# Optimization experiments

Measured on AMD Instinct MI355X. Metric: run time of the kernel, lower is better.

Reference implementation:

```python
import jax, jax.numpy as jnp
import numpy as np

BN_EPS = 1e-5


def setup_inputs() -> dict:
    key = jax.random.key(0)
    ks = jax.random.split(key, 12)
    N, K, C_IN, C_OUT = 50000, 16, 128, 128
    C2 = 2 * C_OUT
    return {
        "features": jax.random.normal(ks[0], (N, C_IN), dtype=jnp.float32),
        "neighbor_idx": jax.random.randint(ks[1], (N, K), 0, N, dtype=jnp.int64),
        "W1": jax.random.normal(ks[2], (C_IN, C2), dtype=jnp.float32) * 0.05,
        "b1": jax.random.normal(ks[3], (C2,), dtype=jnp.float32) * 0.05,
        "gamma": jax.random.uniform(ks[4], (C2,), dtype=jnp.float32, minval=0.5, maxval=1.5),
        "beta": jax.random.normal(ks[5], (C2,), dtype=jnp.float32) * 0.05,
        "run_mean": jax.random.normal(ks[6], (C2,), dtype=jnp.float32) * 0.05,
        "run_var": jax.random.uniform(ks[7], (C2,), dtype=jnp.float32, minval=0.5, maxval=1.5),
        "Ws": jax.random.normal(ks[8], (C2, C2), dtype=jnp.float32) * 0.05,
        "Wm": jax.random.normal(ks[9], (C2, C_OUT), dtype=jnp.float32) * 0.05,
        "bm": jax.random.normal(ks[10], (C_OUT,), dtype=jnp.float32) * 0.05,
    }


def reference(features, neighbor_idx, W1, b1, gamma, beta, run_mean, run_var, Ws, Wm, bm):
    # mlp1: Linear + ReLU (no BN)
    x = jax.nn.relu(features @ W1 + b1)                     # (N, 2C)
    # gather_neighbour: irregular index_select
    g = x[neighbor_idx]                                     # (N, k, 2C)
    # BatchNorm1d over channel dim (inference semantics, running stats)
    inv = gamma * jax.lax.rsqrt(run_var + BN_EPS)
    g = (g - run_mean) * inv + beta                         # (N, k, 2C)
    # AttentivePooling: per-neighbor score linear (no bias), softmax over k
    scores = jax.nn.softmax(g @ Ws, axis=1)                 # (N, k, 2C)
    feat = jnp.sum(scores * g, axis=1)                      # (N, 2C)
    return feat @ Wm + bm                                   # (N, C_out)
```

## Files before the change

kernel.cpp:

```cpp
#include <hip/hip_runtime.h>
#include <cstddef>

#define C_IN  128
#define C2    256
#define C_OUT 128
#define KNBR  16

typedef unsigned short u16;
typedef __attribute__((ext_vector_type(8))) short bf16x8;
typedef __attribute__((ext_vector_type(4))) float f32x4;

__device__ __forceinline__ float bf2f(u16 h) {
    return __uint_as_float(((unsigned int)h) << 16);
}
__device__ __forceinline__ u16 f2bf(float x) {
    unsigned int u = __float_as_uint(x);
    return (u16)((u + 0x7fffu + ((u >> 16) & 1u)) >> 16);
}

__global__ void prep_k(const float* __restrict__ W1, const float* __restrict__ Ws,
                       const float* __restrict__ Wm, u16* __restrict__ W1t,
                       u16* __restrict__ Wst, u16* __restrict__ Wmt)
{
    const int n = blockIdx.x, t = threadIdx.x;
    if (blockIdx.y == 0) {
        if (t < 128) W1t[n * 128 + t] = f2bf(W1[t * 256 + n]);
    } else if (blockIdx.y == 1) {
        Wst[n * 256 + t] = f2bf(Ws[t * 256 + n]);
    } else {
        if (n < 128) Wmt[n * 256 + t] = f2bf(Wm[t * 128 + n]);
    }
}

template<int MODE, bool A_BF16>
__global__ __launch_bounds__(256)
void mfma_gemm(const void* __restrict__ Ap, int lda, int aoff,
               const u16* __restrict__ Bt,
               const float* __restrict__ bias, const float* __restrict__ gamma,
               const float* __restrict__ beta, const float* __restrict__ mean,
               const float* __restrict__ var,
               float* __restrict__ Cf, u16* __restrict__ packed,
               int M, int Kd, int Nc)
{
    __shared__ u16 As[128][40];
    __shared__ u16 Bs[128][40];
    const int tid = threadIdx.x;
    const int w = tid >> 6, l = tid & 63, q = l >> 4, r = l & 15;
    const int wm = w & 1, wn = w >> 1;
    const int m0 = blockIdx.x * 128, n0 = blockIdx.y * 128;

    f32x4 acc[4][4] = {};

    for (int k0 = 0; k0 < Kd; k0 += 32) {
        if (A_BF16) {
            const u16* A = (const u16*)Ap;
            #pragma unroll
            for (int i = 0; i < 2; i++) {
                int idx = tid + i * 256;
                int row = idx >> 2, g = (idx & 3) * 8;
                int gm = m0 + row;
                uint4 v = make_uint4(0u, 0u, 0u, 0u);
                if (gm < M)
                    v = *(const uint4*)(A + (size_t)gm * lda + aoff + k0 + g);
                *(uint4*)&As[row][g] = v;
            }
        } else {
            const float* A = (const float*)Ap;
            #pragma unroll
            for (int i = 0; i < 4; i++) {
                int idx = tid + i * 256;
                int row = idx >> 3, g = (idx & 7) * 4;
                int gm = m0 + row;
                float4 v = make_float4(0.f, 0.f, 0.f, 0.f);
                if (gm < M)
                    v = *(const float4*)(A + (size_t)gm * lda + k0 + g);
                ushort4 h;
                h.x = f2bf(v.x); h.y = f2bf(v.y);
                h.z = f2bf(v.z); h.w = f2bf(v.w);
                *(ushort4*)&As[row][g] = h;
            }
        }
        #pragma unroll
        for (int i = 0; i < 2; i++) {
            int idx = tid + i * 256;
            int row = idx >> 2, g = (idx & 3) * 8;
            *(uint4*)&Bs[row][g] =
                *(const uint4*)(Bt + (size_t)(n0 + row) * Kd + k0 + g);
        }
        __syncthreads();

        bf16x8 af[4], bfr[4];
        #pragma unroll
        for (int i = 0; i < 4; i++)
            af[i] = *(const bf16x8*)&As[wm * 64 + i * 16 + r][q * 8];
        #pragma unroll
        for (int j = 0; j < 4; j++)
            bfr[j] = *(const bf16x8*)&Bs[wn * 64 + j * 16 + r][q * 8];
        #pragma unroll
        for (int i = 0; i < 4; i++)
            #pragma unroll
            for (int j = 0; j < 4; j++)
                acc[i][j] = __builtin_amdgcn_mfma_f32_16x16x32_bf16(
                    af[i], bfr[j], acc[i][j], 0, 0, 0);
        __syncthreads();
    }

    #pragma unroll
    for (int j = 0; j < 4; j++) {
        const int ch = n0 + wn * 64 + j * 16 + r;
        float bi = 0.f, be = 0.f, mu = 0.f, iv = 0.f, bo = 0.f;
        if (MODE == 1) {
            bi = bias[ch]; be = beta[ch]; mu = mean[ch];
            iv = gamma[ch] * rsqrtf(var[ch] + 1e-5f);
        }
        if (MODE == 2) bo = bias[ch];
        #pragma unroll
        for (int i = 0; i < 4; i++) {
            const int mb = m0 + wm * 64 + i * 16 + q * 4;
            #pragma unroll
            for (int p = 0; p < 4; p++) {
                const int m = mb + p;
                if (m >= M) continue;
                float x = acc[i][j][p];
                if (MODE == 1) {
                    x = fmaxf(x + bi, 0.f);
                    x = (x - mu) * iv + be;
                    packed[(size_t)m * 512 + 256 + ch] = f2bf(x);
                } else if (MODE == 0) {
                    packed[(size_t)m * 512 + ch] = f2bf(x);
                } else {
                    Cf[(size_t)m * Nc + ch] = x + bo;
                }
            }
        }
    }
}

__global__ __launch_bounds__(256)
void gather_k(const u16* __restrict__ packed, const int* __restrict__ nidx,
              u16* __restrict__ featb, int N)
{
    __shared__ int rows[4 * KNBR];
    const int tid = threadIdx.x;
    const int p0 = blockIdx.x * 4;

    if (tid < 4 * KNBR) {
        int n = p0 + (tid >> 4);
        rows[tid] = (n < N) ? nidx[n * KNBR + (tid & 15)] : 0;
    }
    __syncthreads();

    const int w = tid >> 6;
    const int l = tid & 63;
    const int p = p0 + w;
    if (p >= N) return;

    ushort4 yh[KNBR], xh[KNBR];
    #pragma unroll
    for (int k = 0; k < KNBR; k++) {
        const size_t base = (size_t)rows[w * KNBR + k] * 512;
        yh[k] = *(const ushort4*)(packed + base + l * 4);
        xh[k] = *(const ushort4*)(packed + base + 256 + l * 4);
    }

    float d0 = 0.f, d1 = 0.f, d2 = 0.f, d3 = 0.f;
    float u0 = 0.f, u1 = 0.f, u2 = 0.f, u3 = 0.f;
    #pragma unroll
    for (int k = 0; k < KNBR; k++) {
        float e0 = __expf(bf2f(yh[k].x));
        float e1 = __expf(bf2f(yh[k].y));
        float e2 = __expf(bf2f(yh[k].z));
        float e3 = __expf(bf2f(yh[k].w));
        d0 += e0; d1 += e1; d2 += e2; d3 += e3;
        u0 = fmaf(e0, bf2f(xh[k].x), u0);
        u1 = fmaf(e1, bf2f(xh[k].y), u1);
        u2 = fmaf(e2, bf2f(xh[k].z), u2);
        u3 = fmaf(e3, bf2f(xh[k].w), u3);
    }
    ushort4 o;
    o.x = f2bf(u0 / d0); o.y = f2bf(u1 / d1);
    o.z = f2bf(u2 / d2); o.w = f2bf(u3 / d3);
    *(ushort4*)(featb + (size_t)p * C2 + l * 4) = o;
}

extern "C" void kernel_launch(void* const* d_in, const int* in_sizes, int n_in,
                              void* d_out, int out_size, void* d_ws, size_t ws_size,
                              hipStream_t stream)
{
    const float* features = (const float*)d_in[0];
    const int*   nidx     = (const int*)d_in[1];
    const float* W1       = (const float*)d_in[2];
    const float* b1       = (const float*)d_in[3];
    const float* gamma    = (const float*)d_in[4];
    const float* beta     = (const float*)d_in[5];
    const float* mean     = (const float*)d_in[6];
    const float* var      = (const float*)d_in[7];
    const float* Ws       = (const float*)d_in[8];
    const float* Wm       = (const float*)d_in[9];
    const float* bm       = (const float*)d_in[10];
    float* out = (float*)d_out;

    const int N = in_sizes[0] / C_IN;

    u16* packed = (u16*)d_ws;
    u16* featb  = packed + (size_t)N * 512;
    u16* W1t    = featb + (size_t)N * 256;
    u16* Wst    = W1t + 256 * 128;
    u16* Wmt    = Wst + 256 * 256;

    prep_k<<<dim3(256, 3), 256, 0, stream>>>(W1, Ws, Wm, W1t, Wst, Wmt);

    const int MT = (N + 127) / 128;

    mfma_gemm<1, false><<<dim3(MT, 2), 256, 0, stream>>>(
        features, C_IN, 0, W1t, b1, gamma, beta, mean, var,
        nullptr, packed, N, C_IN, C2);
    mfma_gemm<0, true><<<dim3(MT, 2), 256, 0, stream>>>(
        packed, 512, 256, Wst, nullptr, nullptr, nullptr, nullptr, nullptr,
        nullptr, packed, N, C2, C2);
    gather_k<<<(N + 3) / 4, 256, 0, stream>>>(packed, nidx, featb, N);
    mfma_gemm<2, true><<<dim3(MT, 1), 256, 0, stream>>>(
        featb, C2, 0, Wmt, bm, nullptr, nullptr, nullptr, nullptr,
        out, nullptr, N, C2, C_OUT);
}
```

Baseline: 274.2 us.

## Interleave exp-scores with BN features and precompute exp in the GEMM epilogue

The packed buffer now interleaves groups of four exp(score) values with the matching four BN-normalized features. Each gather thread fetches both with a single 16-byte load per neighbor instead of two 8-byte loads. The exp is computed once per row in the score GEMM epilogue instead of once per neighbor in the gather, and a separate contiguous copy of the BN features feeds the score GEMM. The GEMM K-tile also grows from 32 to 64. Costs include an extra write of the BN features, exp values rounded to bf16, and the gather output buffer aliased onto the output tensor.

```diff
diff --git a/kernel.cpp b/kernel.cpp
--- a/kernel.cpp
+++ b/kernel.cpp
@@ -34,16 +34,16 @@
 
 template<int MODE, bool A_BF16>
 __global__ __launch_bounds__(256)
-void mfma_gemm(const void* __restrict__ Ap, int lda, int aoff,
+void mfma_gemm(const void* __restrict__ Ap, int lda,
                const u16* __restrict__ Bt,
                const float* __restrict__ bias, const float* __restrict__ gamma,
                const float* __restrict__ beta, const float* __restrict__ mean,
                const float* __restrict__ var,
                float* __restrict__ Cf, u16* __restrict__ packed,
-               int M, int Kd, int Nc)
-{
-    __shared__ u16 As[128][40];
-    __shared__ u16 Bs[128][40];
+               u16* __restrict__ xbn_c, int M, int Kd, int Nc)
+{
+    __shared__ u16 As[128][72];
+    __shared__ u16 Bs[128][72];
     const int tid = threadIdx.x;
     const int w = tid >> 6, l = tid & 63, q = l >> 4, r = l & 15;
     const int wm = w & 1, wn = w >> 1;
@@ -51,25 +51,25 @@
 
     f32x4 acc[4][4] = {};
 
-    for (int k0 = 0; k0 < Kd; k0 += 32) {
+    for (int k0 = 0; k0 < Kd; k0 += 64) {
         if (A_BF16) {
             const u16* A = (const u16*)Ap;
             #pragma unroll
-            for (int i = 0; i < 2; i++) {
+            for (int i = 0; i < 4; i++) {
                 int idx = tid + i * 256;
-                int row = idx >> 2, g = (idx & 3) * 8;
+                int row = idx >> 3, g = (idx & 7) * 8;
                 int gm = m0 + row;
                 uint4 v = make_uint4(0u, 0u, 0u, 0u);
                 if (gm < M)
-                    v = *(const uint4*)(A + (size_t)gm * lda + aoff + k0 + g);
+                    v = *(const uint4*)(A + (size_t)gm * lda + k0 + g);
                 *(uint4*)&As[row][g] = v;
             }
         } else {
             const float* A = (const float*)Ap;
             #pragma unroll
-            for (int i = 0; i < 4; i++) {
+            for (int i = 0; i < 8; i++) {
                 int idx = tid + i * 256;
-                int row = idx >> 3, g = (idx & 7) * 4;
+                int row = idx >> 4, g = (idx & 15) * 4;
                 int gm = m0 + row;
                 float4 v = make_float4(0.f, 0.f, 0.f, 0.f);
                 if (gm < M)
@@ -81,27 +81,30 @@
             }
         }
         #pragma unroll
-        for (int i = 0; i < 2; i++) {
+        for (int i = 0; i < 4; i++) {
             int idx = tid + i * 256;
-            int row = idx >> 2, g = (idx & 3) * 8;
+            int row = idx >> 3, g = (idx & 7) * 8;
             *(uint4*)&Bs[row][g] =
                 *(const uint4*)(Bt + (size_t)(n0 + row) * Kd + k0 + g);
         }
         __syncthreads();
 
-        bf16x8 af[4], bfr[4];
         #pragma unroll
-        for (int i = 0; i < 4; i++)
-            af[i] = *(const bf16x8*)&As[wm * 64 + i * 16 + r][q * 8];
-        #pragma unroll
-        for (int j = 0; j < 4; j++)
-            bfr[j] = *(const bf16x8*)&Bs[wn * 64 + j * 16 + r][q * 8];
-        #pragma unroll
-        for (int i = 0; i < 4; i++)
+        for (int h = 0; h < 2; h++) {
+            bf16x8 af[4], bfr[4];
+            #pragma unroll
+            for (int i = 0; i < 4; i++)
+                af[i] = *(const bf16x8*)&As[wm * 64 + i * 16 + r][h * 32 + q * 8];
             #pragma unroll
             for (int j = 0; j < 4; j++)
-                acc[i][j] = __builtin_amdgcn_mfma_f32_16x16x32_bf16(
-                    af[i], bfr[j], acc[i][j], 0, 0, 0);
+                bfr[j] = *(const bf16x8*)&Bs[wn * 64 + j * 16 + r][h * 32 + q * 8];
+            #pragma unroll
+            for (int i = 0; i < 4; i++)
+                #pragma unroll
+                for (int j = 0; j < 4; j++)
+                    acc[i][j] = __builtin_amdgcn_mfma_f32_16x16x32_bf16(
+                        af[i], bfr[j], acc[i][j], 0, 0, 0);
+        }
         __syncthreads();
     }
 
@@ -114,6 +117,7 @@
             iv = gamma[ch] * rsqrtf(var[ch] + 1e-5f);
         }
         if (MODE == 2) bo = bias[ch];
+        const int goff = (ch >> 2) * 8 + (ch & 3);
         #pragma unroll
         for (int i = 0; i < 4; i++) {
             const int mb = m0 + wm * 64 + i * 16 + q * 4;
@@ -125,9 +129,11 @@
                 if (MODE == 1) {
                     x = fmaxf(x + bi, 0.f);
                     x = (x - mu) * iv + be;
-                    packed[(size_t)m * 512 + 256 + ch] = f2bf(x);
+                    u16 hx = f2bf(x);
+                    packed[(size_t)m * 512 + goff + 4] = hx;
+                    xbn_c[(size_t)m * 256 + ch] = hx;
                 } else if (MODE == 0) {
-                    packed[(size_t)m * 512 + ch] = f2bf(x);
+                    packed[(size_t)m * 512 + goff] = f2bf(__expf(x));
                 } else {
                     Cf[(size_t)m * Nc + ch] = x + bo;
                 }
@@ -155,27 +161,28 @@
     const int p = p0 + w;
     if (p >= N) return;
 
-    ushort4 yh[KNBR], xh[KNBR];
+    uint4 v[KNBR];
     #pragma unroll
-    for (int k = 0; k < KNBR; k++) {
-        const size_t base = (size_t)rows[w * KNBR + k] * 512;
-        yh[k] = *(const ushort4*)(packed + base + l * 4);
-        xh[k] = *(const ushort4*)(packed + base + 256 + l * 4);
-    }
+    for (int k = 0; k < KNBR; k++)
+        v[k] = *(const uint4*)(packed + (size_t)rows[w * KNBR + k] * 512 + l * 8);
 
     float d0 = 0.f, d1 = 0.f, d2 = 0.f, d3 = 0.f;
     float u0 = 0.f, u1 = 0.f, u2 = 0.f, u3 = 0.f;
     #pragma unroll
     for (int k = 0; k < KNBR; k++) {
-        float e0 = __expf(bf2f(yh[k].x));
-        float e1 = __expf(bf2f(yh[k].y));
-        float e2 = __expf(bf2f(yh[k].z));
-        float e3 = __expf(bf2f(yh[k].w));
+        float e0 = __uint_as_float(v[k].x << 16);
+        float e1 = __uint_as_float(v[k].x & 0xffff0000u);
+        float e2 = __uint_as_float(v[k].y << 16);
+        float e3 = __uint_as_float(v[k].y & 0xffff0000u);
+        float x0 = __uint_as_float(v[k].z << 16);
+        float x1 = __uint_as_float(v[k].z & 0xffff0000u);
+        float x2 = __uint_as_float(v[k].w << 16);
+        float x3 = __uint_as_float(v[k].w & 0xffff0000u);
         d0 += e0; d1 += e1; d2 += e2; d3 += e3;
-        u0 = fmaf(e0, bf2f(xh[k].x), u0);
-        u1 = fmaf(e1, bf2f(xh[k].y), u1);
-        u2 = fmaf(e2, bf2f(xh[k].z), u2);
-        u3 = fmaf(e3, bf2f(xh[k].w), u3);
+        u0 = fmaf(e0, x0, u0);
+        u1 = fmaf(e1, x1, u1);
+        u2 = fmaf(e2, x2, u2);
+        u3 = fmaf(e3, x3, u3);
     }
     ushort4 o;
     o.x = f2bf(u0 / d0); o.y = f2bf(u1 / d1);
@@ -203,23 +210,24 @@
     const int N = in_sizes[0] / C_IN;
 
     u16* packed = (u16*)d_ws;
-    u16* featb  = packed + (size_t)N * 512;
-    u16* W1t    = featb + (size_t)N * 256;
+    u16* xbn_c  = packed + (size_t)N * 512;
+    u16* W1t    = xbn_c + (size_t)N * 256;
     u16* Wst    = W1t + 256 * 128;
     u16* Wmt    = Wst + 256 * 256;
+    u16* featb = (u16*)d_out;
 
     prep_k<<<dim3(256, 3), 256, 0, stream>>>(W1, Ws, Wm, W1t, Wst, Wmt);
 
     const int MT = (N + 127) / 128;
 
     mfma_gemm<1, false><<<dim3(MT, 2), 256, 0, stream>>>(
-        features, C_IN, 0, W1t, b1, gamma, beta, mean, var,
-        nullptr, packed, N, C_IN, C2);
+        features, C_IN, W1t, b1, gamma, beta, mean, var,
+        nullptr, packed, xbn_c, N, C_IN, C2);
     mfma_gemm<0, true><<<dim3(MT, 2), 256, 0, stream>>>(
-        packed, 512, 256, Wst, nullptr, nullptr, nullptr, nullptr, nullptr,
-        nullptr, packed, N, C2, C2);
+        xbn_c, C2, Wst, nullptr, nullptr, nullptr, nullptr, nullptr,
+        nullptr, packed, nullptr, N, C2, C2);
     gather_k<<<(N + 3) / 4, 256, 0, stream>>>(packed, nidx, featb, N);
     mfma_gemm<2, true><<<dim3(MT, 1), 256, 0, stream>>>(
-        featb, C2, 0, Wmt, bm, nullptr, nullptr, nullptr, nullptr,
-        out, nullptr, N, C2, C_OUT);
-}
+        featb, C2, Wmt, bm, nullptr, nullptr, nullptr, nullptr,
+        out, nullptr, nullptr, N, C2, C_OUT);
+}
```

Result: slower. 292.9 us (+6.8%).

## Use persistent LDS-resident-weight GEMM kernels and precompute exp before gather

Applied to the files above, without the earlier changes.

Replaces the tiled 128x128 GEMM template with three persistent kernels: x_k, ey_k and out_k. Each loads its full transposed weight matrix into LDS once per block, then loops waves over 16-row tiles, reading A fragments straight from global memory. The exponent of the attention scores is now computed once per row in the score GEMM epilogue rather than 16 times per neighbour inside the gather, and the BN affine is folded into a single fma. The pooled bf16 features are staged in the output buffer instead of a separate workspace. This relies on the large LDS allocations fitting and on each wave reading its rows before overwriting them in place.

```diff
diff --git a/kernel.cpp b/kernel.cpp
--- a/kernel.cpp
+++ b/kernel.cpp
@@ -32,105 +32,149 @@
     }
 }
 
-template<int MODE, bool A_BF16>
-__global__ __launch_bounds__(256)
-void mfma_gemm(const void* __restrict__ Ap, int lda, int aoff,
-               const u16* __restrict__ Bt,
-               const float* __restrict__ bias, const float* __restrict__ gamma,
-               const float* __restrict__ beta, const float* __restrict__ mean,
-               const float* __restrict__ var,
-               float* __restrict__ Cf, u16* __restrict__ packed,
-               int M, int Kd, int Nc)
-{
-    __shared__ u16 As[128][40];
-    __shared__ u16 Bs[128][40];
-    const int tid = threadIdx.x;
-    const int w = tid >> 6, l = tid & 63, q = l >> 4, r = l & 15;
-    const int wm = w & 1, wn = w >> 1;
-    const int m0 = blockIdx.x * 128, n0 = blockIdx.y * 128;
-
-    f32x4 acc[4][4] = {};
-
-    for (int k0 = 0; k0 < Kd; k0 += 32) {
-        if (A_BF16) {
-            const u16* A = (const u16*)Ap;
-            #pragma unroll
-            for (int i = 0; i < 2; i++) {
-                int idx = tid + i * 256;
-                int row = idx >> 2, g = (idx & 3) * 8;
-                int gm = m0 + row;
-                uint4 v = make_uint4(0u, 0u, 0u, 0u);
-                if (gm < M)
-                    v = *(const uint4*)(A + (size_t)gm * lda + aoff + k0 + g);
-                *(uint4*)&As[row][g] = v;
-            }
-        } else {
-            const float* A = (const float*)Ap;
-            #pragma unroll
-            for (int i = 0; i < 4; i++) {
-                int idx = tid + i * 256;
-                int row = idx >> 3, g = (idx & 7) * 4;
-                int gm = m0 + row;
-                float4 v = make_float4(0.f, 0.f, 0.f, 0.f);
-                if (gm < M)
-                    v = *(const float4*)(A + (size_t)gm * lda + k0 + g);
-                ushort4 h;
-                h.x = f2bf(v.x); h.y = f2bf(v.y);
-                h.z = f2bf(v.z); h.w = f2bf(v.w);
-                *(ushort4*)&As[row][g] = h;
-            }
-        }
-        #pragma unroll
-        for (int i = 0; i < 2; i++) {
-            int idx = tid + i * 256;
-            int row = idx >> 2, g = (idx & 3) * 8;
-            *(uint4*)&Bs[row][g] =
-                *(const uint4*)(Bt + (size_t)(n0 + row) * Kd + k0 + g);
-        }
-        __syncthreads();
-
-        bf16x8 af[4], bfr[4];
-        #pragma unroll
-        for (int i = 0; i < 4; i++)
-            af[i] = *(const bf16x8*)&As[wm * 64 + i * 16 + r][q * 8];
-        #pragma unroll
-        for (int j = 0; j < 4; j++)
-            bfr[j] = *(const bf16x8*)&Bs[wn * 64 + j * 16 + r][q * 8];
-        #pragma unroll
-        for (int i = 0; i < 4; i++)
-            #pragma unroll
-            for (int j = 0; j < 4; j++)
-                acc[i][j] = __builtin_amdgcn_mfma_f32_16x16x32_bf16(
-                    af[i], bfr[j], acc[i][j], 0, 0, 0);
-        __syncthreads();
-    }
-
-    #pragma unroll
-    for (int j = 0; j < 4; j++) {
-        const int ch = n0 + wn * 64 + j * 16 + r;
-        float bi = 0.f, be = 0.f, mu = 0.f, iv = 0.f, bo = 0.f;
-        if (MODE == 1) {
-            bi = bias[ch]; be = beta[ch]; mu = mean[ch];
-            iv = gamma[ch] * rsqrtf(var[ch] + 1e-5f);
-        }
-        if (MODE == 2) bo = bias[ch];
-        #pragma unroll
-        for (int i = 0; i < 4; i++) {
-            const int mb = m0 + wm * 64 + i * 16 + q * 4;
+
+__global__ __launch_bounds__(1024, 4)
+void x_k(const float* __restrict__ F, const u16* __restrict__ W1t,
+         const float* __restrict__ b1, const float* __restrict__ gamma,
+         const float* __restrict__ beta, const float* __restrict__ mean,
+         const float* __restrict__ var, u16* __restrict__ packed, int N)
+{
+    __shared__ u16 WL[256][136];
+    __shared__ float cb1[256], civ[256], cbb[256];
+    const int tid = threadIdx.x;
+    #pragma unroll
+    for (int i = 0; i < 4; i++) {
+        int idx = tid + i * 1024;
+        int row = idx >> 4, g = (idx & 15) * 8;
+        *(uint4*)&WL[row][g] = *(const uint4*)(W1t + (size_t)row * C_IN + g);
+    }
+    if (tid < 256) {
+        float iv = gamma[tid] * rsqrtf(var[tid] + 1e-5f);
+        civ[tid] = iv;
+        cbb[tid] = beta[tid] - mean[tid] * iv;
+        cb1[tid] = b1[tid];
+    }
+    __syncthreads();
+
+    const int wv = tid >> 6, l = tid & 63, q = l >> 4, r = l & 15;
+    const int ntiles = (N + 15) / 16;
+    for (int t = blockIdx.x * 16 + wv; t < ntiles; t += gridDim.x * 16) {
+        const int m0 = t * 16;
+        const int arow = min(m0 + r, N - 1);
+        f32x4 acc[16] = {};
+        #pragma unroll
+        for (int kk = 0; kk < 4; kk++) {
+            float4 a0 = *(const float4*)(F + (size_t)arow * C_IN + kk * 32 + q * 8);
+            float4 a1 = *(const float4*)(F + (size_t)arow * C_IN + kk * 32 + q * 8 + 4);
+            bf16x8 af;
+            af[0] = (short)f2bf(a0.x); af[1] = (short)f2bf(a0.y);
+            af[2] = (short)f2bf(a0.z); af[3] = (short)f2bf(a0.w);
+            af[4] = (short)f2bf(a1.x); af[5] = (short)f2bf(a1.y);
+            af[6] = (short)f2bf(a1.z); af[7] = (short)f2bf(a1.w);
+            #pragma unroll
+            for (int n = 0; n < 16; n++) {
+                bf16x8 bf = *(const bf16x8*)&WL[n * 16 + r][kk * 32 + q * 8];
+                acc[n] = __builtin_amdgcn_mfma_f32_16x16x32_bf16(af, bf, acc[n], 0, 0, 0);
+            }
+        }
+        #pragma unroll
+        for (int n = 0; n < 16; n++) {
+            const int ch = n * 16 + r;
+            const float bi = cb1[ch], iv = civ[ch], bb = cbb[ch];
             #pragma unroll
             for (int p = 0; p < 4; p++) {
-                const int m = mb + p;
-                if (m >= M) continue;
-                float x = acc[i][j][p];
-                if (MODE == 1) {
-                    x = fmaxf(x + bi, 0.f);
-                    x = (x - mu) * iv + be;
-                    packed[(size_t)m * 512 + 256 + ch] = f2bf(x);
-                } else if (MODE == 0) {
-                    packed[(size_t)m * 512 + ch] = f2bf(x);
-                } else {
-                    Cf[(size_t)m * Nc + ch] = x + bo;
+                const int m = m0 + q * 4 + p;
+                if (m < N) {
+                    float x = fmaxf(acc[n][p] + bi, 0.f);
+                    packed[(size_t)m * 512 + 256 + ch] = f2bf(fmaf(x, iv, bb));
                 }
+            }
+        }
+    }
+}
+
+__global__ __launch_bounds__(1024, 4)
+void ey_k(const u16* __restrict__ packed_r, const u16* __restrict__ Wst,
+          u16* __restrict__ packed_w, int N)
+{
+    __shared__ u16 WL[256][264];
+    const int tid = threadIdx.x;
+    #pragma unroll
+    for (int i = 0; i < 8; i++) {
+        int idx = tid + i * 1024;
+        int row = idx >> 5, g = (idx & 31) * 8;
+        *(uint4*)&WL[row][g] = *(const uint4*)(Wst + (size_t)row * C2 + g);
+    }
+    __syncthreads();
+
+    const int wv = tid >> 6, l = tid & 63, q = l >> 4, r = l & 15;
+    const int ntiles = (N + 15) / 16;
+    for (int t = blockIdx.x * 16 + wv; t < ntiles; t += gridDim.x * 16) {
+        const int m0 = t * 16;
+        const int arow = min(m0 + r, N - 1);
+        f32x4 acc[16] = {};
+        #pragma unroll
+        for (int kk = 0; kk < 8; kk++) {
+            bf16x8 af = *(const bf16x8*)(packed_r + (size_t)arow * 512 + 256
+                                         + kk * 32 + q * 8);
+            #pragma unroll
+            for (int n = 0; n < 16; n++) {
+                bf16x8 bf = *(const bf16x8*)&WL[n * 16 + r][kk * 32 + q * 8];
+                acc[n] = __builtin_amdgcn_mfma_f32_16x16x32_bf16(af, bf, acc[n], 0, 0, 0);
+            }
+        }
+        #pragma unroll
+        for (int n = 0; n < 16; n++) {
+            const int ch = n * 16 + r;
+            #pragma unroll
+            for (int p = 0; p < 4; p++) {
+                const int m = m0 + q * 4 + p;
+                if (m < N)
+                    packed_w[(size_t)m * 512 + ch] = f2bf(__expf(acc[n][p]));
+            }
+        }
+    }
+}
+
+__global__ __launch_bounds__(1024, 4)
+void out_k(const u16* featb, const u16* __restrict__ Wmt,
+           const float* __restrict__ bm, float* out, int N)
+{
+    __shared__ u16 WL[128][264];
+    __shared__ float cbm[128];
+    const int tid = threadIdx.x;
+    #pragma unroll
+    for (int i = 0; i < 4; i++) {
+        int idx = tid + i * 1024;
+        int row = idx >> 5, g = (idx & 31) * 8;
+        *(uint4*)&WL[row][g] = *(const uint4*)(Wmt + (size_t)row * C2 + g);
+    }
+    if (tid < 128) cbm[tid] = bm[tid];
+    __syncthreads();
+
+    const int wv = tid >> 6, l = tid & 63, q = l >> 4, r = l & 15;
+    const int ntiles = (N + 15) / 16;
+    for (int t = blockIdx.x * 16 + wv; t < ntiles; t += gridDim.x * 16) {
+        const int m0 = t * 16;
+        const int arow = min(m0 + r, N - 1);
+        f32x4 acc[8] = {};
+        #pragma unroll
+        for (int kk = 0; kk < 8; kk++) {
+            bf16x8 af = *(const bf16x8*)(featb + (size_t)arow * C2 + kk * 32 + q * 8);
+            #pragma unroll
+            for (int n = 0; n < 8; n++) {
+                bf16x8 bf = *(const bf16x8*)&WL[n * 16 + r][kk * 32 + q * 8];
+                acc[n] = __builtin_amdgcn_mfma_f32_16x16x32_bf16(af, bf, acc[n], 0, 0, 0);
+            }
+        }
+        #pragma unroll
+        for (int n = 0; n < 8; n++) {
+            const int ch = n * 16 + r;
+            const float bo = cbm[ch];
+            #pragma unroll
+            for (int p = 0; p < 4; p++) {
+                const int m = m0 + q * 4 + p;
+                if (m < N) out[(size_t)m * C_OUT + ch] = acc[n][p] + bo;
             }
         }
     }
@@ -155,11 +199,11 @@
     const int p = p0 + w;
     if (p >= N) return;
 
-    ushort4 yh[KNBR], xh[KNBR];
+    ushort4 eh[KNBR], xh[KNBR];
     #pragma unroll
     for (int k = 0; k < KNBR; k++) {
         const size_t base = (size_t)rows[w * KNBR + k] * 512;
-        yh[k] = *(const ushort4*)(packed + base + l * 4);
+        eh[k] = *(const ushort4*)(packed + base + l * 4);
         xh[k] = *(const ushort4*)(packed + base + 256 + l * 4);
     }
 
@@ -167,10 +211,8 @@
     float u0 = 0.f, u1 = 0.f, u2 = 0.f, u3 = 0.f;
     #pragma unroll
     for (int k = 0; k < KNBR; k++) {
-        float e0 = __expf(bf2f(yh[k].x));
-        float e1 = __expf(bf2f(yh[k].y));
-        float e2 = __expf(bf2f(yh[k].z));
-        float e3 = __expf(bf2f(yh[k].w));
+        float e0 = bf2f(eh[k].x), e1 = bf2f(eh[k].y);
+        float e2 = bf2f(eh[k].z), e3 = bf2f(eh[k].w);
         d0 += e0; d1 += e1; d2 += e2; d3 += e3;
         u0 = fmaf(e0, bf2f(xh[k].x), u0);
         u1 = fmaf(e1, bf2f(xh[k].y), u1);
@@ -203,23 +245,16 @@
     const int N = in_sizes[0] / C_IN;
 
     u16* packed = (u16*)d_ws;
-    u16* featb  = packed + (size_t)N * 512;
-    u16* W1t    = featb + (size_t)N * 256;
+    u16* W1t    = packed + (size_t)N * 512;
     u16* Wst    = W1t + 256 * 128;
     u16* Wmt    = Wst + 256 * 256;
+    u16* featb = (u16*)d_out;
 
     prep_k<<<dim3(256, 3), 256, 0, stream>>>(W1, Ws, Wm, W1t, Wst, Wmt);
 
-    const int MT = (N + 127) / 128;
-
-    mfma_gemm<1, false><<<dim3(MT, 2), 256, 0, stream>>>(
-        features, C_IN, 0, W1t, b1, gamma, beta, mean, var,
-        nullptr, packed, N, C_IN, C2);
-    mfma_gemm<0, true><<<dim3(MT, 2), 256, 0, stream>>>(
-        packed, 512, 256, Wst, nullptr, nullptr, nullptr, nullptr, nullptr,
-        nullptr, packed, N, C2, C2);
+    x_k<<<256, 1024, 0, stream>>>(features, W1t, b1, gamma, beta, mean, var,
+                                  packed, N);
+    ey_k<<<256, 1024, 0, stream>>>(packed, Wst, packed, N);
     gather_k<<<(N + 3) / 4, 256, 0, stream>>>(packed, nidx, featb, N);
-    mfma_gemm<2, true><<<dim3(MT, 1), 256, 0, stream>>>(
-        featb, C2, 0, Wmt, bm, nullptr, nullptr, nullptr, nullptr,
-        out, nullptr, N, C2, C_OUT);
-}
+    out_k<<<256, 1024, 0, stream>>>(featb, Wmt, bm, out, N);
+}
```

After: 627.3 us. 2.29x slower.
